# Kernel optimization log

Measured on AMD Instinct MI355X. Metric: run time of the kernel, lower is better.

The kernel has to match this reference:

```python
import jax, jax.numpy as jnp
import numpy as np

DIM = 192; HEADS = 6; HD = DIM // HEADS; SCALE = HD ** -0.5
WS = (4, 8, 8); SS = (2, 4, 4)
NW = WS[0] * WS[1] * WS[2]  # tokens per window = 256
HIDDEN = 768; RANK1 = 384; RANK2 = 96

def _rel_index():
    Wd, Wh, Ww = WS
    coords = np.stack(np.meshgrid(np.arange(Wd), np.arange(Wh), np.arange(Ww), indexing='ij')).reshape(3, -1)
    rel = (coords[:, :, None] - coords[:, None, :]).transpose(1, 2, 0)
    rel = rel + np.array([Wd - 1, Wh - 1, Ww - 1])
    rel[:, :, 0] *= (2 * Wh - 1) * (2 * Ww - 1)
    rel[:, :, 1] *= 2 * Ww - 1
    return rel.sum(-1)  # (NW, NW) int

REL_IDX = jnp.asarray(_rel_index())

def _attn_mask(B, D, H, W):
    # static numpy computation (D,H,W are python ints) -> constant under jit
    img = np.zeros((B, D, H, W), np.float32); cnt = 0
    for d in range(0, D, WS[0]):
        for h in range(0, H, WS[1]):
            for w in range(0, W, WS[2]):
                img[:, d:d + WS[0], h:h + WS[1], w:w + WS[2]] = cnt; cnt += 1
    if any(s > 0 for s in SS):
        img = np.roll(img, (-SS[0], -SS[1], -SS[2]), axis=(1, 2, 3))
    mw = img.reshape(B, D // WS[0], WS[0], H // WS[1], WS[1], W // WS[2], WS[2]).transpose(0, 1, 3, 5, 2, 4, 6).reshape(-1, NW)
    diff = mw[:, :, None] - mw[:, None, :]
    return jnp.asarray(np.where(diff != 0, -100.0, 0.0).astype(np.float32))  # (B*nW, NW, NW)

def _ln(x, g, b):
    mu = x.mean(-1, keepdims=True)
    var = ((x - mu) ** 2).mean(-1, keepdims=True)
    return (x - mu) / jnp.sqrt(var + 1e-5) * g + b

def setup_inputs() -> dict:
    key = jax.random.key(0)
    ks = jax.random.split(key, 16)
    B, D, H, W = 1, 16, 64, 64
    N = D * H * W
    s = 0.02
    return {
        'x': jax.random.normal(ks[0], (B, N, DIM), jnp.float32),
        'norm1_g': jnp.ones((DIM,), jnp.float32), 'norm1_b': jnp.zeros((DIM,), jnp.float32),
        'qkv_w': jax.random.normal(ks[1], (DIM, 3 * DIM), jnp.float32) * s,
        'qkv_b': jnp.zeros((3 * DIM,), jnp.float32),
        'rel_bias': jax.random.normal(ks[2], (1575, HEADS), jnp.float32) * s,
        'proj_w': jax.random.normal(ks[3], (DIM, DIM), jnp.float32) * s,
        'proj_b': jnp.zeros((DIM,), jnp.float32),
        'norm2_g': jnp.ones((DIM,), jnp.float32), 'norm2_b': jnp.zeros((DIM,), jnp.float32),
        'fc1_A': jax.random.normal(ks[4], (DIM, RANK1), jnp.float32) * s,
        'fc1_Bw': jax.random.normal(ks[5], (RANK1, HIDDEN), jnp.float32) * s,
        'fc1_Bb': jnp.zeros((HIDDEN,), jnp.float32),
        'dw_w': jax.random.normal(ks[6], (HIDDEN, 1, 3, 3, 3), jnp.float32) * s,
        'dw_b': jnp.zeros((HIDDEN,), jnp.float32),
        'fc2_A': jax.random.normal(ks[7], (HIDDEN, RANK2), jnp.float32) * s,
        'fc2_Bw': jax.random.normal(ks[8], (RANK2, DIM), jnp.float32) * s,
        'fc2_Bb': jnp.zeros((DIM,), jnp.float32),
        'D': D, 'H': H, 'W': W,
    }

def reference(x, norm1_g, norm1_b, qkv_w, qkv_b, rel_bias, proj_w, proj_b,
              norm2_g, norm2_b, fc1_A, fc1_Bw, fc1_Bb, dw_w, dw_b,
              fc2_A, fc2_Bw, fc2_Bb, D, H, W):
    B, N, C = x.shape
    Wd, Wh, Ww = WS
    shortcut = x
    # --- shifted-window attention (NB: original repo never rolls x; only the mask is shifted) ---
    h = _ln(x, norm1_g, norm1_b).reshape(B, D, H, W, C)
    xw = h.reshape(B, D // Wd, Wd, H // Wh, Wh, W // Ww, Ww, C)
    xw = xw.transpose(0, 1, 3, 5, 2, 4, 6, 7).reshape(-1, NW, C)  # (B*nW, NW, C)
    qkv = (xw @ qkv_w + qkv_b).reshape(-1, NW, 3, HEADS, HD).transpose(2, 0, 3, 1, 4)
    q, k, v = qkv[0] * SCALE, qkv[1], qkv[2]           # (B*nW, heads, NW, hd)
    attn = jnp.einsum('bhnd,bhmd->bhnm', q, k)
    bias = rel_bias[REL_IDX].transpose(2, 0, 1)[None]  # (1, heads, NW, NW)
    mask = _attn_mask(B, D, H, W)                      # (B*nW, NW, NW)
    attn = jax.nn.softmax(attn + bias + mask[:, None], axis=-1)
    out = jnp.einsum('bhnm,bhmd->bhnd', attn, v).transpose(0, 2, 1, 3).reshape(-1, NW, C)
    out = out @ proj_w + proj_b
    out = out.reshape(B, D // Wd, H // Wh, W // Ww, Wd, Wh, Ww, C)
    out = out.transpose(0, 1, 4, 2, 5, 3, 6, 7).reshape(B, N, C)
    x = shortcut + out
    # --- MixFFN3D: low-rank fc1 -> depthwise conv3d -> GELU -> low-rank fc2 ---
    h = _ln(x, norm2_g, norm2_b)
    h = (h @ fc1_A) @ fc1_Bw + fc1_Bb                 # (B, N, HIDDEN)
    h = h.transpose(0, 2, 1).reshape(B, HIDDEN, D, H, W)
    h = jax.lax.conv_general_dilated(h, dw_w, (1, 1, 1), [(1, 1), (1, 1), (1, 1)],
                                     feature_group_count=HIDDEN,
                                     dimension_numbers=('NCDHW', 'OIDHW', 'NCDHW'))
    h = h + dw_b[None, :, None, None, None]
    h = jax.nn.gelu(h, approximate=False)
    h = h.reshape(B, HIDDEN, N).transpose(0, 2, 1)
    h = (h @ fc2_A) @ fc2_Bw + fc2_Bb                 # (B, N, DIM)
    return x + h
```

## Files before the change

kernel.cpp:

```cpp
#include <hip/hip_runtime.h>
#include <hip/hip_bf16.h>

typedef __hip_bfloat16 bf16;
typedef __attribute__((ext_vector_type(8))) short short8;
typedef __attribute__((ext_vector_type(4))) float f32x4;

#define N_TOK 65536
#define C_DIM 192
#define SCALE 0.17677669529663687f

__device__ __forceinline__ float b2f(bf16 v) { return __bfloat162float(v); }
__device__ __forceinline__ bf16 f2b(float v) { return __float2bfloat16(v); }
__device__ __forceinline__ float ldA(const void* p, size_t i, int f32) {
  return f32 ? ((const float*)p)[i] : b2f(((const bf16*)p)[i]);
}
__device__ __forceinline__ float s2f(short s) { union { short s; bf16 b; } u; u.s = s; return b2f(u.b); }

__global__ void detect_kernel(const unsigned short* __restrict__ xh, int* __restrict__ flag) {
  if (threadIdx.x == 0) {
    int crazy = 0;
    for (int i = 0; i < 256; ++i) {
      int e = (xh[i] >> 7) & 0xFF;
      if (e >= 0xF0 || (e >= 1 && e <= 0x60)) ++crazy;
    }
    *flag = (crazy >= 16) ? 1 : 0;
  }
}

__global__ __launch_bounds__(256) void prep_kernel(
    const void* __restrict__ qkv_w, bf16* __restrict__ QKVT,
    const void* __restrict__ proj_w, bf16* __restrict__ PROJT,
    const void* __restrict__ fc1_A, bf16* __restrict__ FC1AT,
    const void* __restrict__ fc1_Bw, bf16* __restrict__ FC1BT,
    const void* __restrict__ fc2_A, bf16* __restrict__ FC2AT,
    const void* __restrict__ fc2_Bw, bf16* __restrict__ FC2BT,
    const void* __restrict__ dw_w, float* __restrict__ DWT,
    const int* __restrict__ flag) {
  int f32 = *flag;
  int b = blockIdx.x;
  const void* in; bf16* out; int K, N, base;
  if (b < 432)       { in = qkv_w;  out = QKVT;  K = 192; N = 576; base = 0; }
  else if (b < 576)  { in = proj_w; out = PROJT; K = 192; N = 192; base = 432; }
  else if (b < 864)  { in = fc1_A;  out = FC1AT; K = 192; N = 384; base = 576; }
  else if (b < 2016) { in = fc1_Bw; out = FC1BT; K = 384; N = 768; base = 864; }
  else if (b < 2304) { in = fc2_A;  out = FC2AT; K = 768; N = 96;  base = 2016; }
  else if (b < 2376) { in = fc2_Bw; out = FC2BT; K = 96;  N = 192; base = 2304; }
  else {
    int idx = (b - 2376) * 256 + threadIdx.x;
    int tap = idx / 768, c = idx - tap * 768;
    DWT[idx] = ldA(dw_w, (size_t)c * 27 + tap, f32);
    return;
  }
  int idx = (b - base) * 256 + threadIdx.x;
  int n = idx / K, k = idx - n * K;
  out[idx] = f2b(ldA(in, (size_t)k * N + n, f32));
}

__global__ __launch_bounds__(256) void ln_kernel(const void* __restrict__ x,
    const void* __restrict__ g, const void* __restrict__ b, bf16* __restrict__ out,
    int windowize, int xIsBf16Fixed, const int* __restrict__ flag) {
  int wf32 = *flag;
  int f32 = xIsBf16Fixed ? 0 : wf32;
  int token = blockIdx.x * 4 + (threadIdx.x >> 6);
  int lane = threadIdx.x & 63;
  size_t base = (size_t)token * C_DIM;
  float v0 = ldA(x, base + lane, f32);
  float v1 = ldA(x, base + lane + 64, f32);
  float v2 = ldA(x, base + lane + 128, f32);
  float s = v0 + v1 + v2;
  float s2 = v0 * v0 + v1 * v1 + v2 * v2;
  #pragma unroll
  for (int o = 32; o > 0; o >>= 1) { s += __shfl_xor(s, o, 64); s2 += __shfl_xor(s2, o, 64); }
  float mu = s * (1.f / 192.f);
  float var = s2 * (1.f / 192.f) - mu * mu;
  float rstd = rsqrtf(var + 1e-5f);
  int row = token;
  if (windowize) {
    int d = token >> 12, h = (token >> 6) & 63, w = token & 63;
    int win = ((d >> 2) << 6) + ((h >> 3) << 3) + (w >> 3);
    int t = ((d & 3) << 6) + ((h & 7) << 3) + (w & 7);
    row = win * 256 + t;
  }
  bf16* po = out + (size_t)row * C_DIM;
  po[lane]       = f2b((v0 - mu) * rstd * ldA(g, lane, wf32)       + ldA(b, lane, wf32));
  po[lane + 64]  = f2b((v1 - mu) * rstd * ldA(g, lane + 64, wf32)  + ldA(b, lane + 64, wf32));
  po[lane + 128] = f2b((v2 - mu) * rstd * ldA(g, lane + 128, wf32) + ldA(b, lane + 128, wf32));
}

__global__ __launch_bounds__(256) void mfma_gemm(const bf16* __restrict__ A,
    const bf16* __restrict__ BT, const void* __restrict__ bias,
    const void* __restrict__ res, void* __restrict__ out,
    int Nc, int K, int ldk, int mode, const int* __restrict__ flag) {
  int f32 = *flag;
  __shared__ short As[128 * 40];
  __shared__ short Bs[64 * 40];
  int tid = threadIdx.x;
  int wave = tid >> 6, lane = tid & 63;
  int wm = wave >> 1, wn = wave & 1;
  int lr = lane & 15, quad = lane >> 4;
  int ncb = gridDim.x;
  int flat = blockIdx.x + ncb * blockIdx.y;
  int group = flat / (8 * ncb);
  int r = flat - group * 8 * ncb;
  int rowBase = (group * 8 + (r & 7)) * 128;
  int colBase = (r >> 3) * 64;
  f32x4 acc[4][2];
  #pragma unroll
  for (int i = 0; i < 4; ++i)
    #pragma unroll
    for (int j = 0; j < 2; ++j) acc[i][j] = f32x4{0.f, 0.f, 0.f, 0.f};

  for (int k0 = 0; k0 < K; k0 += 32) {
    #pragma unroll
    for (int it = 0; it < 2; ++it) {
      int idx = tid + it * 256;
      int row = idx >> 2, kc = (idx & 3) * 8;
      uint4 v = *(const uint4*)(A + (size_t)(rowBase + row) * K + k0 + kc);
      *(uint4*)&As[row * 40 + kc] = v;
    }
    {
      int n = tid >> 2, kc = (tid & 3) * 8;
      uint4 v = uint4{0u, 0u, 0u, 0u};
      if (colBase + n < Nc)
        v = *(const uint4*)(BT + (size_t)(colBase + n) * ldk + k0 + kc);
      *(uint4*)&Bs[n * 40 + kc] = v;
    }
    __syncthreads();
    short8 af[4], bf[2];
    #pragma unroll
    for (int i = 0; i < 4; ++i)
      af[i] = *(const short8*)&As[(wm * 64 + i * 16 + lr) * 40 + quad * 8];
    #pragma unroll
    for (int j = 0; j < 2; ++j)
      bf[j] = *(const short8*)&Bs[(wn * 32 + j * 16 + lr) * 40 + quad * 8];
    #pragma unroll
    for (int i = 0; i < 4; ++i)
      #pragma unroll
      for (int j = 0; j < 2; ++j)
        acc[i][j] = __builtin_amdgcn_mfma_f32_16x16x32_bf16(af[i], bf[j], acc[i][j], 0, 0, 0);
    __syncthreads();
  }

  #pragma unroll
  for (int i = 0; i < 4; ++i) {
    #pragma unroll
    for (int j = 0; j < 2; ++j) {
      #pragma unroll
      for (int r4 = 0; r4 < 4; ++r4) {
        int row = rowBase + wm * 64 + i * 16 + quad * 4 + r4;
        int c = colBase + wn * 32 + j * 16 + lr;
        if (c >= Nc) continue;
        float v = acc[i][j][r4];
        if (bias) v += ldA(bias, c, f32);
        if (mode == 0) {
          ((bf16*)out)[(size_t)row * Nc + c] = f2b(v);
        } else if (mode == 1) {
          float o = b2f(((const bf16*)res)[(size_t)row * Nc + c]) + v;
          if (f32) ((float*)out)[(size_t)row * Nc + c] = o;
          else     ((bf16*)out)[(size_t)row * Nc + c] = f2b(o);
        } else {
          int win = row >> 8, t = row & 255;
          int d = ((win >> 6) << 2) + (t >> 6);
          int h = (((win >> 3) & 7) << 3) + ((t >> 3) & 7);
          int w = ((win & 7) << 3) + (t & 7);
          int n = (d << 12) + (h << 6) + w;
          ((bf16*)out)[(size_t)n * C_DIM + c] = f2b(ldA(res, (size_t)n * C_DIM + c, f32) + v);
        }
      }
    }
  }
}

__global__ __launch_bounds__(256) void attn_mfma_kernel(const bf16* __restrict__ qkvr,
    const void* __restrict__ rel_bias, bf16* __restrict__ out,
    const int* __restrict__ flag) {
  int f32 = *flag;
  __shared__ bf16 sK[256 * 40];
  __shared__ bf16 sVT[32 * 264];
  __shared__ bf16 sP[4][64 * 40];
  __shared__ float sb[1575];
  __shared__ int  sgb[256];
  int head = blockIdx.x, win = blockIdx.y;
  const bf16* base = qkvr + (size_t)win * 256 * 576;
  int qoff = head * 32, koff = 192 + head * 32, voff = 384 + head * 32;
  int tid = threadIdx.x;
  int wave = tid >> 6, lane = tid & 63;
  int lr = lane & 15, quad = lane >> 4;

  #pragma unroll
  for (int it = 0; it < 4; ++it) {
    int idx = tid + it * 256;
    int tok = idx >> 2, kc = (idx & 3) * 8;
    uint4 v = *(const uint4*)(base + (size_t)tok * 576 + koff + kc);
    *(uint4*)&sK[tok * 40 + kc] = v;
  }
  for (int idx = tid; idx < 8192; idx += 256) {
    int tok = idx >> 5, hd = idx & 31;
    sVT[hd * 264 + tok] = base[(size_t)tok * 576 + voff + hd];
  }
  for (int idx = tid; idx < 1575; idx += 256) sb[idx] = ldA(rel_bias, (size_t)idx * 6 + head, f32);
  {
    int t = tid & 255;
    int d = ((win >> 6) << 2) + (t >> 6);
    int h = (((win >> 3) & 7) << 3) + ((t >> 3) & 7);
    int w = ((win & 7) << 3) + (t & 7);
    int d2 = (d + 2) & 15, h2 = (h + 4) & 63, w2 = (w + 4) & 63;
    int g = ((d2 >> 2) << 6) + ((h2 >> 3) << 3) + (w2 >> 3);
    int td = t >> 6, th = (t >> 3) & 7, tw = t & 7;
    int bse = (td * 15 + th) * 15 + tw;
    sgb[t] = (g << 12) | bse;
  }
  __syncthreads();

  int wm = wave * 64;
  short8 aq[4];
  #pragma unroll
  for (int i = 0; i < 4; ++i)
    aq[i] = *(const short8*)(base + (size_t)(wm + i * 16 + lr) * 576 + qoff + quad * 8);
  int rinfo[16];
  #pragma unroll
  for (int i = 0; i < 4; ++i)
    #pragma unroll
    for (int r = 0; r < 4; ++r)
      rinfo[i * 4 + r] = sgb[wm + i * 16 + quad * 4 + r];

  f32x4 acc_o[4][2], acc_l[4];
  #pragma unroll
  for (int i = 0; i < 4; ++i) {
    acc_l[i] = f32x4{0.f, 0.f, 0.f, 0.f};
    #pragma unroll
    for (int j = 0; j < 2; ++j) acc_o[i][j] = f32x4{0.f, 0.f, 0.f, 0.f};
  }
  short8 bones;
  #pragma unroll
  for (int j = 0; j < 8; ++j) bones[j] = (lr == 0) ? (short)0x3F80 : (short)0;

  for (int c = 0; c < 8; ++c) {
    short8 bk[2];
    #pragma unroll
    for (int jt = 0; jt < 2; ++jt)
      bk[jt] = *(const short8*)&sK[(c * 32 + jt * 16 + lr) * 40 + quad * 8];
    f32x4 s[4][2];
    #pragma unroll
    for (int i = 0; i < 4; ++i)
      #pragma unroll
      for (int jt = 0; jt < 2; ++jt) {
        s[i][jt] = f32x4{0.f, 0.f, 0.f, 0.f};
        s[i][jt] = __builtin_amdgcn_mfma_f32_16x16x32_bf16(aq[i], bk[jt], s[i][jt], 0, 0, 0);
      }
    int cinfo[2];
    #pragma unroll
    for (int jt = 0; jt < 2; ++jt) cinfo[jt] = sgb[c * 32 + jt * 16 + lr];
    #pragma unroll
    for (int i = 0; i < 4; ++i)
      #pragma unroll
      for (int jt = 0; jt < 2; ++jt)
        #pragma unroll
        for (int r = 0; r < 4; ++r) {
          int ri = rinfo[i * 4 + r], ci = cinfo[jt];
          float sc = s[i][jt][r] * SCALE + sb[(ri & 0xFFF) - (ci & 0xFFF) + 787];
          float p = ((ri >> 12) == (ci >> 12)) ? __expf(sc) : 0.f;
          sP[wave][(i * 16 + quad * 4 + r) * 40 + jt * 16 + lr] = f2b(p);
        }
    short8 ap[4];
    #pragma unroll
    for (int i = 0; i < 4; ++i)
      ap[i] = *(const short8*)&sP[wave][(i * 16 + lr) * 40 + quad * 8];
    short8 bv[2];
    #pragma unroll
    for (int jh = 0; jh < 2; ++jh)
      bv[jh] = *(const short8*)&sVT[(jh * 16 + lr) * 264 + c * 32 + quad * 8];
    #pragma unroll
    for (int i = 0; i < 4; ++i) {
      #pragma unroll
      for (int jh = 0; jh < 2; ++jh)
        acc_o[i][jh] = __builtin_amdgcn_mfma_f32_16x16x32_bf16(ap[i], bv[jh], acc_o[i][jh], 0, 0, 0);
      acc_l[i] = __builtin_amdgcn_mfma_f32_16x16x32_bf16(ap[i], bones, acc_l[i], 0, 0, 0);
    }
  }
  #pragma unroll
  for (int i = 0; i < 4; ++i) {
    #pragma unroll
    for (int r = 0; r < 4; ++r) {
      float l = __shfl(acc_l[i][r], lane & 48, 64);
      float inv = 1.f / l;
      int t = wm + i * 16 + quad * 4 + r;
      bf16* po = out + (size_t)(win * 256 + t) * C_DIM + head * 32;
      po[lr]      = f2b(acc_o[i][0][r] * inv);
      po[16 + lr] = f2b(acc_o[i][1][r] * inv);
    }
  }
}

__global__ __launch_bounds__(256) void dwconv8w4_kernel(const bf16* __restrict__ in,
    const float* __restrict__ wT, const void* __restrict__ wb, bf16* __restrict__ out,
    const int* __restrict__ flag) {
  int f32 = *flag;
  int cpx = gridDim.x >> 3;
  int vb = (blockIdx.x & 7) * cpx + (blockIdx.x >> 3);
  int idx = vb * 256 + threadIdx.x;
  int n4 = idx / 96, g = idx - n4 * 96;
  int c0 = g * 8;
  int d = n4 >> 10, h = (n4 >> 4) & 63, w0 = (n4 & 15) << 2;
  const bf16* inb = in + c0;
  float acc[4][8];
  {
    float bias[8];
    #pragma unroll
    for (int e = 0; e < 8; ++e) bias[e] = ldA(wb, c0 + e, f32);
    #pragma unroll
    for (int t = 0; t < 4; ++t)
      #pragma unroll
      for (int e = 0; e < 8; ++e) acc[t][e] = bias[e];
  }
  #pragma unroll
  for (int kd = 0; kd < 3; ++kd) {
    int dd = d + kd - 1;
    if ((unsigned)dd >= 16u) continue;
    #pragma unroll
    for (int kh = 0; kh < 3; ++kh) {
      int hh = h + kh - 1;
      if ((unsigned)hh >= 64u) continue;
      int rowbase = (dd << 12) + (hh << 6);
      float xf[6][8];
      #pragma unroll
      for (int j = 0; j < 6; ++j) {
        int ww = w0 + j - 1;
        short8 xv = short8{0, 0, 0, 0, 0, 0, 0, 0};
        if ((unsigned)ww < 64u)
          xv = *(const short8*)(inb + (size_t)(rowbase + ww) * 768);
        #pragma unroll
        for (int e = 0; e < 8; ++e) xf[j][e] = s2f(xv[e]);
      }
      #pragma unroll
      for (int kw = 0; kw < 3; ++kw) {
        int tap = kd * 9 + kh * 3 + kw;
        f32x4 wlo = *(const f32x4*)(wT + tap * 768 + c0);
        f32x4 whi = *(const f32x4*)(wT + tap * 768 + c0 + 4);
        float wf[8];
        #pragma unroll
        for (int e = 0; e < 4; ++e) { wf[e] = wlo[e]; wf[e + 4] = whi[e]; }
        #pragma unroll
        for (int t = 0; t < 4; ++t)
          #pragma unroll
          for (int e = 0; e < 8; ++e)
            acc[t][e] += xf[t + kw][e] * wf[e];
      }
    }
  }
  #pragma unroll
  for (int t = 0; t < 4; ++t) {
    bf16* po = out + (size_t)((d << 12) + (h << 6) + w0 + t) * 768 + c0;
    #pragma unroll
    for (int e = 0; e < 8; ++e) {
      float s = acc[t][e];
      po[e] = f2b(0.5f * s * (1.f + erff(s * 0.70710678118654752f)));
    }
  }
}

extern "C" void kernel_launch(void* const* d_in, const int* in_sizes, int n_in,
                              void* d_out, int out_size, void* d_ws, size_t ws_size,
                              hipStream_t stream) {
  const void* x      = d_in[0];
  const void* n1g    = d_in[1];
  const void* n1b    = d_in[2];
  const void* qkv_w  = d_in[3];
  const void* qkv_b  = d_in[4];
  const void* relb   = d_in[5];
  const void* proj_w = d_in[6];
  const void* proj_b = d_in[7];
  const void* n2g    = d_in[8];
  const void* n2b    = d_in[9];
  const void* fc1_A  = d_in[10];
  const void* fc1_Bw = d_in[11];
  const void* fc1_Bb = d_in[12];
  const void* dw_w   = d_in[13];
  const void* dw_b   = d_in[14];
  const void* fc2_A  = d_in[15];
  const void* fc2_Bw = d_in[16];
  const void* fc2_Bb = d_in[17];

  char* ws = (char*)d_ws;
  bf16* SCR  = (bf16*)d_out;
  bf16* X1   = (bf16*)(ws);
  bf16* QKVR = (bf16*)(ws + (size_t)24 * 1048576);
  bf16* T1   = (bf16*)(ws + (size_t)24 * 1048576);
  bf16* F2   = (bf16*)(ws + (size_t)24 * 1048576);
  bf16* F1   = (bf16*)(ws + (size_t)120 * 1048576);
  bf16* T2bf = (bf16*)(ws + (size_t)216 * 1048576);
  bf16* QKVT  = (bf16*)(ws + (size_t)228 * 1048576);
  bf16* PROJT = (bf16*)(ws + (size_t)229 * 1048576);
  bf16* FC1AT = (bf16*)(ws + (size_t)230 * 1048576);
  bf16* FC1BT = (bf16*)(ws + (size_t)231 * 1048576);
  bf16* FC2AT = (bf16*)(ws + (size_t)233 * 1048576);
  bf16* FC2BT = (bf16*)(ws + (size_t)234 * 1048576);
  float* DWT  = (float*)(ws + (size_t)235 * 1048576);
  int* FLAG   = (int*)(ws + (size_t)255 * 1048576);

  detect_kernel<<<1, 64, 0, stream>>>((const unsigned short*)x, FLAG);
  prep_kernel<<<2457, 256, 0, stream>>>(qkv_w, QKVT, proj_w, PROJT, fc1_A, FC1AT,
                                        fc1_Bw, FC1BT, fc2_A, FC2AT, fc2_Bw, FC2BT,
                                        dw_w, DWT, FLAG);
  ln_kernel<<<N_TOK / 4, 256, 0, stream>>>(x, n1g, n1b, SCR, 1, 0, FLAG);
  mfma_gemm<<<dim3(9, 512), 256, 0, stream>>>(SCR, QKVT, qkv_b, nullptr, QKVR,
                                              576, 192, 192, 0, FLAG);
  attn_mfma_kernel<<<dim3(6, 256), 256, 0, stream>>>(QKVR, relb, SCR, FLAG);
  mfma_gemm<<<dim3(3, 512), 256, 0, stream>>>(SCR, PROJT, proj_b, x, X1,
                                              192, 192, 192, 3, FLAG);
  ln_kernel<<<N_TOK / 4, 256, 0, stream>>>(X1, n2g, n2b, SCR, 0, 1, FLAG);
  mfma_gemm<<<dim3(6, 512), 256, 0, stream>>>(SCR, FC1AT, nullptr, nullptr, T1,
                                              384, 192, 192, 0, FLAG);
  mfma_gemm<<<dim3(12, 512), 256, 0, stream>>>(T1, FC1BT, fc1_Bb, nullptr, F1,
                                               768, 384, 384, 0, FLAG);
  dwconv8w4_kernel<<<6144, 256, 0, stream>>>(F1, DWT, dw_b, F2, FLAG);
  mfma_gemm<<<dim3(2, 512), 256, 0, stream>>>(F2, FC2AT, nullptr, nullptr, T2bf,
                                              96, 768, 768, 0, FLAG);
  mfma_gemm<<<dim3(3, 512), 256, 0, stream>>>(T2bf, FC2BT, fc2_Bb, X1, d_out,
                                              192, 96, 96, 1, FLAG);
}
```

Measured before the change: 753.8 us.

## Widen GEMM K-tile to 96, store dwconv weights as bf16, drop block swizzle

The MFMA GEMM now stages a 96-wide K slice per iteration instead of 32, cutting the number of barrier pairs per tile by a factor of three at the cost of larger shared memory. The depthwise conv weights are stored as bf16 rather than fp32, halving weight load traffic but rounding the weights. The dwconv block-index swizzle is removed in favour of linear block order. All GEMM K values used here (192, 384) are multiples of 96, but the fc2 GEMMs with K=768 and K=96 also need to divide, which they do.

```diff
diff --git a/kernel.cpp b/kernel.cpp
--- a/kernel.cpp
+++ b/kernel.cpp
@@ -34,7 +34,7 @@
     const void* __restrict__ fc1_Bw, bf16* __restrict__ FC1BT,
     const void* __restrict__ fc2_A, bf16* __restrict__ FC2AT,
     const void* __restrict__ fc2_Bw, bf16* __restrict__ FC2BT,
-    const void* __restrict__ dw_w, float* __restrict__ DWT,
+    const void* __restrict__ dw_w, bf16* __restrict__ DWT,
     const int* __restrict__ flag) {
   int f32 = *flag;
   int b = blockIdx.x;
@@ -48,7 +48,7 @@
   else {
     int idx = (b - 2376) * 256 + threadIdx.x;
     int tap = idx / 768, c = idx - tap * 768;
-    DWT[idx] = ldA(dw_w, (size_t)c * 27 + tap, f32);
+    DWT[idx] = f2b(ldA(dw_w, (size_t)c * 27 + tap, f32));
     return;
   }
   int idx = (b - base) * 256 + threadIdx.x;
@@ -92,8 +92,8 @@
     const void* __restrict__ res, void* __restrict__ out,
     int Nc, int K, int ldk, int mode, const int* __restrict__ flag) {
   int f32 = *flag;
-  __shared__ short As[128 * 40];
-  __shared__ short Bs[64 * 40];
+  __shared__ short As[128 * 104];
+  __shared__ short Bs[64 * 104];
   int tid = threadIdx.x;
   int wave = tid >> 6, lane = tid & 63;
   int wm = wave >> 1, wn = wave & 1;
@@ -110,34 +110,39 @@
     #pragma unroll
     for (int j = 0; j < 2; ++j) acc[i][j] = f32x4{0.f, 0.f, 0.f, 0.f};
 
-  for (int k0 = 0; k0 < K; k0 += 32) {
-    #pragma unroll
-    for (int it = 0; it < 2; ++it) {
-      int idx = tid + it * 256;
-      int row = idx >> 2, kc = (idx & 3) * 8;
+  for (int k0 = 0; k0 < K; k0 += 96) {
+    #pragma unroll
+    for (int it = 0; it < 6; ++it) {
+      int u = tid + it * 256;
+      int row = u / 12, kc = (u - row * 12) * 8;
       uint4 v = *(const uint4*)(A + (size_t)(rowBase + row) * K + k0 + kc);
-      *(uint4*)&As[row * 40 + kc] = v;
-    }
-    {
-      int n = tid >> 2, kc = (tid & 3) * 8;
+      *(uint4*)&As[row * 104 + kc] = v;
+    }
+    #pragma unroll
+    for (int it = 0; it < 3; ++it) {
+      int u = tid + it * 256;
+      int n = u / 12, kc = (u - n * 12) * 8;
       uint4 v = uint4{0u, 0u, 0u, 0u};
       if (colBase + n < Nc)
         v = *(const uint4*)(BT + (size_t)(colBase + n) * ldk + k0 + kc);
-      *(uint4*)&Bs[n * 40 + kc] = v;
+      *(uint4*)&Bs[n * 104 + kc] = v;
     }
     __syncthreads();
-    short8 af[4], bf[2];
-    #pragma unroll
-    for (int i = 0; i < 4; ++i)
-      af[i] = *(const short8*)&As[(wm * 64 + i * 16 + lr) * 40 + quad * 8];
-    #pragma unroll
-    for (int j = 0; j < 2; ++j)
-      bf[j] = *(const short8*)&Bs[(wn * 32 + j * 16 + lr) * 40 + quad * 8];
-    #pragma unroll
-    for (int i = 0; i < 4; ++i)
+    #pragma unroll
+    for (int kk = 0; kk < 3; ++kk) {
+      short8 af[4], bf[2];
+      #pragma unroll
+      for (int i = 0; i < 4; ++i)
+        af[i] = *(const short8*)&As[(wm * 64 + i * 16 + lr) * 104 + kk * 32 + quad * 8];
       #pragma unroll
       for (int j = 0; j < 2; ++j)
-        acc[i][j] = __builtin_amdgcn_mfma_f32_16x16x32_bf16(af[i], bf[j], acc[i][j], 0, 0, 0);
+        bf[j] = *(const short8*)&Bs[(wn * 32 + j * 16 + lr) * 104 + kk * 32 + quad * 8];
+      #pragma unroll
+      for (int i = 0; i < 4; ++i)
+        #pragma unroll
+        for (int j = 0; j < 2; ++j)
+          acc[i][j] = __builtin_amdgcn_mfma_f32_16x16x32_bf16(af[i], bf[j], acc[i][j], 0, 0, 0);
+    }
     __syncthreads();
   }
 
@@ -293,12 +298,10 @@
 }
 
 __global__ __launch_bounds__(256) void dwconv8w4_kernel(const bf16* __restrict__ in,
-    const float* __restrict__ wT, const void* __restrict__ wb, bf16* __restrict__ out,
+    const bf16* __restrict__ wT, const void* __restrict__ wb, bf16* __restrict__ out,
     const int* __restrict__ flag) {
   int f32 = *flag;
-  int cpx = gridDim.x >> 3;
-  int vb = (blockIdx.x & 7) * cpx + (blockIdx.x >> 3);
-  int idx = vb * 256 + threadIdx.x;
+  int idx = blockIdx.x * 256 + threadIdx.x;
   int n4 = idx / 96, g = idx - n4 * 96;
   int c0 = g * 8;
   int d = n4 >> 10, h = (n4 >> 4) & 63, w0 = (n4 & 15) << 2;
@@ -335,11 +338,10 @@
       #pragma unroll
       for (int kw = 0; kw < 3; ++kw) {
         int tap = kd * 9 + kh * 3 + kw;
-        f32x4 wlo = *(const f32x4*)(wT + tap * 768 + c0);
-        f32x4 whi = *(const f32x4*)(wT + tap * 768 + c0 + 4);
+        short8 wv = *(const short8*)(wT + tap * 768 + c0);
         float wf[8];
         #pragma unroll
-        for (int e = 0; e < 4; ++e) { wf[e] = wlo[e]; wf[e + 4] = whi[e]; }
+        for (int e = 0; e < 8; ++e) wf[e] = s2f(wv[e]);
         #pragma unroll
         for (int t = 0; t < 4; ++t)
           #pragma unroll
@@ -395,7 +397,7 @@
   bf16* FC1BT = (bf16*)(ws + (size_t)231 * 1048576);
   bf16* FC2AT = (bf16*)(ws + (size_t)233 * 1048576);
   bf16* FC2BT = (bf16*)(ws + (size_t)234 * 1048576);
-  float* DWT  = (float*)(ws + (size_t)235 * 1048576);
+  bf16* DWT   = (bf16*)(ws + (size_t)235 * 1048576);
   int* FLAG   = (int*)(ws + (size_t)255 * 1048576);
 
   detect_kernel<<<1, 64, 0, stream>>>((const unsigned short*)x, FLAG);
```

Result: faster. 732.9 us (-2.8%).
